# Optimization experiments

Measured on AMD Instinct MI355X. Metric: run time of the kernel, lower is better.

The kernel has to match this reference:

```python
import jax, jax.numpy as jnp
import numpy as np

D_MODEL = 2048
N_HEADS = 32
N_KV = 8
D_K = D_MODEL // N_HEADS  # 64
N_REP = N_HEADS // N_KV   # 4


def setup_inputs() -> dict:
    key = jax.random.key(0)
    ks = jax.random.split(key, 5)
    B, T = 2, 2048
    s = 0.02
    return {
        "x": jax.random.normal(ks[0], (B, T, D_MODEL), dtype=jnp.float32),
        "Wq": jax.random.normal(ks[1], (D_MODEL, D_MODEL), dtype=jnp.float32) * s,
        "Wk": jax.random.normal(ks[2], (N_KV * D_K, D_MODEL), dtype=jnp.float32) * s,
        "Wv": jax.random.normal(ks[3], (N_KV * D_K, D_MODEL), dtype=jnp.float32) * s,
        "Wo": jax.random.normal(ks[4], (D_MODEL, D_MODEL), dtype=jnp.float32) * s,
    }


def reference(x, Wq, Wk, Wv, Wo):
    B, T, C = x.shape
    # projections (torch Linear: x @ W.T)
    Q = (x @ Wq.T).reshape(B, T, N_KV, N_REP, D_K)  # group query heads by kv group
    K = (x @ Wk.T).reshape(B, T, N_KV, D_K)
    V = (x @ Wv.T).reshape(B, T, N_KV, D_K)
    scale = 1.0 / jnp.sqrt(jnp.asarray(D_K, dtype=x.dtype))
    # scores: (B, n_kv, n_rep, T, T) == repeated-KV scores without materializing repeats
    scores = jnp.einsum('btgrd,bsgd->bgrts', Q, K) * scale
    causal_mask = jnp.triu(jnp.ones((T, T), dtype=bool), k=1)
    scores = jnp.where(causal_mask, -jnp.inf, scores)
    attn = jax.nn.softmax(scores, axis=-1)
    out = jnp.einsum('bgrts,bsgd->btgrd', attn, V).reshape(B, T, C)
    return out @ Wo.T
```

## Files before the change

kernel.cpp:

```cpp
#include <hip/hip_runtime.h>
#include <hip/hip_bf16.h>

typedef __attribute__((ext_vector_type(8))) short bf16x8;
typedef __attribute__((ext_vector_type(4))) float floatx4;

constexpr int D_MODEL = 2048;
constexpr int N_HEADS = 32;
constexpr int N_KV    = 8;
constexpr int B_      = 2;
constexpr int T_      = 2048;
constexpr int BT      = B_ * T_;
constexpr int NQKV    = 3072;

constexpr float Q_SCALE = 0.18033688011112042f;

__device__ __forceinline__ unsigned short f2bf(float f) {
    __hip_bfloat16 h = __float2bfloat16(f);
    return *reinterpret_cast<unsigned short*>(&h);
}

__device__ __forceinline__ void gll16(const void* g, void* l) {
    typedef const __attribute__((address_space(1))) unsigned int* gp_t;
    typedef __attribute__((address_space(3))) unsigned int* lp_t;
    __builtin_amdgcn_global_load_lds((gp_t)g, (lp_t)l, 16, 0, 0);
}

__global__ __launch_bounds__(256) void cvt_all(
        const float* __restrict__ x,  const float* __restrict__ wq,
        const float* __restrict__ wk, const float* __restrict__ wv,
        unsigned short* __restrict__ dst) {
    size_t i4 = (size_t)blockIdx.x * 256 + threadIdx.x;
    size_t e = i4 * 4;
    const float* src; size_t off;
    if (e < 8388608)        { src = x;  off = 0; }
    else if (e < 12582912)  { src = wq; off = 8388608; }
    else if (e < 13631488)  { src = wk; off = 12582912; }
    else                    { src = wv; off = 13631488; }
    float4 f = *reinterpret_cast<const float4*>(src + (e - off));
    unsigned short u[4] = {f2bf(f.x), f2bf(f.y), f2bf(f.z), f2bf(f.w)};
    reinterpret_cast<uint2*>(dst)[i4] = *reinterpret_cast<const uint2*>(u);
}

__global__ __launch_bounds__(256) void cvt_bf16(
        const float* __restrict__ src, unsigned short* __restrict__ dst, int n4) {
    int i = blockIdx.x * 256 + threadIdx.x;
    if (i < n4) {
        float4 f = reinterpret_cast<const float4*>(src)[i];
        unsigned short u[4] = {f2bf(f.x), f2bf(f.y), f2bf(f.z), f2bf(f.w)};
        reinterpret_cast<uint2*>(dst)[i] = *reinterpret_cast<const uint2*>(u);
    }
}

template<bool C_F32, bool SCALEQ>
__global__ __launch_bounds__(256) void gemm128(
        const unsigned short* __restrict__ A,
        const unsigned short* __restrict__ Bb,
        void* __restrict__ Cp,
        int M, int N, int K) {
    __shared__ unsigned short As[128 * 64];
    __shared__ unsigned short Bs[128 * 64];
    const int t = threadIdx.x;
    const int wave = t >> 6, lane = t & 63;
    const int l16 = lane & 15, quad = lane >> 4;
    const int wm = (wave & 1) * 64, wn = (wave >> 1) * 64;
    const int mtile = blockIdx.y * 128, ntile = blockIdx.x * 128;

    floatx4 acc[4][4] = {};

    for (int k0 = 0; k0 < K; k0 += 64) {
        __syncthreads();
#pragma unroll
        for (int c = 0; c < 4; c++) {
            int s = (c * 4 + wave) * 64 + lane;
            int row = s >> 3, k8 = (s & 7) ^ (row & 7);
            gll16(&A[(size_t)(mtile + row) * K + k0 + k8 * 8], &As[(c * 4 + wave) * 512]);
            gll16(&Bb[(size_t)(ntile + row) * K + k0 + k8 * 8], &Bs[(c * 4 + wave) * 512]);
        }
        __syncthreads();
#pragma unroll
        for (int kc = 0; kc < 2; kc++) {
            bf16x8 af[4], bfr[4];
#pragma unroll
            for (int i = 0; i < 4; i++) {
                int arow = wm + i * 16 + l16;
                af[i] = *reinterpret_cast<const bf16x8*>(
                    &As[(arow * 8 + ((kc * 4 + quad) ^ (arow & 7))) * 8]);
                int brow = wn + i * 16 + l16;
                bfr[i] = *reinterpret_cast<const bf16x8*>(
                    &Bs[(brow * 8 + ((kc * 4 + quad) ^ (brow & 7))) * 8]);
            }
#pragma unroll
            for (int i = 0; i < 4; i++)
#pragma unroll
                for (int jn = 0; jn < 4; jn++)
                    acc[i][jn] = __builtin_amdgcn_mfma_f32_16x16x32_bf16(
                        af[i], bfr[jn], acc[i][jn], 0, 0, 0);
        }
    }
    float cscale = (SCALEQ && ntile < 2048) ? Q_SCALE : 1.0f;
#pragma unroll
    for (int i = 0; i < 4; i++)
#pragma unroll
        for (int jn = 0; jn < 4; jn++)
#pragma unroll
            for (int r = 0; r < 4; r++) {
                int row = mtile + wm + i * 16 + quad * 4 + r;
                int col = ntile + wn + jn * 16 + l16;
                if constexpr (C_F32)
                    ((float*)Cp)[(size_t)row * N + col] = acc[i][jn][r];
                else
                    ((unsigned short*)Cp)[(size_t)row * N + col] =
                        f2bf(acc[i][jn][r] * cscale);
            }
}

__global__ __launch_bounds__(256) void vtrans(
        const unsigned short* __restrict__ QKV,
        unsigned short* __restrict__ Vt) {
    __shared__ unsigned short Ts[64][72];
    const int tb = blockIdx.x * 64;
    const int bg = blockIdx.y;
    const int b = bg >> 3, g = bg & 7;
    const int t = threadIdx.x;
#pragma unroll
    for (int it = 0; it < 2; it++) {
        int row = (t >> 3) + it * 32;
        int sl = t & 7;
        *reinterpret_cast<uint4*>(&Ts[row][sl * 8]) =
            *reinterpret_cast<const uint4*>(
                &QKV[(size_t)(b * T_ + tb + row) * NQKV + 2560 + g * 64 + sl * 8]);
    }
    __syncthreads();
#pragma unroll
    for (int it = 0; it < 2; it++) {
        int d = (t >> 3) + it * 32;
        int ks = t & 7;
        unsigned short u[8];
#pragma unroll
        for (int j = 0; j < 8; j++) u[j] = Ts[ks * 8 + j][d];
        *reinterpret_cast<uint4*>(&Vt[((size_t)bg * 64 + d) * T_ + tb + ks * 8]) =
            *reinterpret_cast<const uint4*>(u);
    }
}

__global__ __launch_bounds__(256, 2) void attn5(
        const unsigned short* __restrict__ QKV,
        const unsigned short* __restrict__ Vt,
        unsigned short* __restrict__ O) {
    __shared__ unsigned short Ks[64 * 64];
    __shared__ unsigned short Vs[64 * 64];
    __shared__ unsigned short Ps[4][32 * 72];
    const int j  = blockIdx.x;
    const int bh = blockIdx.y;
    const int b = bh >> 5, h = bh & 31;
    const int g = h >> 2;
    const int t = threadIdx.x, wave = t >> 6, lane = t & 63;
    const int l16 = lane & 15, quad = lane >> 4;

    bf16x8 ones;
#pragma unroll
    for (int i = 0; i < 8; i++) ones[i] = (short)0x3F80;

    for (int pp = 0; pp < 2; pp++) {
        const int qtl = pp ? (15 - j) : j;
        const int q0  = qtl * 128;
        const int qlo = q0 + wave * 32;

        bf16x8 qf[2][2];
#pragma unroll
        for (int qb = 0; qb < 2; qb++) {
            const unsigned short* qptr =
                QKV + (size_t)(b * T_ + qlo + qb * 16 + l16) * NQKV + h * 64;
            qf[qb][0] = *reinterpret_cast<const bf16x8*>(qptr + quad * 8);
            qf[qb][1] = *reinterpret_cast<const bf16x8*>(qptr + 32 + quad * 8);
        }

        floatx4 o[2][4] = {};
        floatx4 lacc[2] = {};

        const int nkt = 2 * qtl + 2;
        for (int kt = 0; kt < nkt; kt++) {
            const int kb = kt * 64;
            __syncthreads();
#pragma unroll
            for (int c = 0; c < 2; c++) {
                int s = (c * 4 + wave) * 64 + lane;
                int row = s >> 3, k8 = (s & 7) ^ (row & 7);
                gll16(&QKV[(size_t)(b * T_ + kb + row) * NQKV + 2048 + g * 64 + k8 * 8],
                      &Ks[(c * 4 + wave) * 512]);
                gll16(&Vt[((size_t)(b * 8 + g) * 64 + row) * T_ + kb + k8 * 8],
                      &Vs[(c * 4 + wave) * 512]);
            }
            __syncthreads();

            if (kb > qlo + 31) continue;
            const bool needmask = (kb + 63 > qlo);

#pragma unroll
            for (int km = 0; km < 4; km++) {
                int krow = km * 16 + l16;
                bf16x8 k0 = *reinterpret_cast<const bf16x8*>(
                    &Ks[(krow * 8 + (quad ^ (krow & 7))) * 8]);
                bf16x8 k1 = *reinterpret_cast<const bf16x8*>(
                    &Ks[(krow * 8 + ((4 + quad) ^ (krow & 7))) * 8]);
#pragma unroll
                for (int qb = 0; qb < 2; qb++) {
                    floatx4 z = {};
                    z = __builtin_amdgcn_mfma_f32_16x16x32_bf16(k0, qf[qb][0], z, 0, 0, 0);
                    z = __builtin_amdgcn_mfma_f32_16x16x32_bf16(k1, qf[qb][1], z, 0, 0, 0);
                    unsigned short u[4];
                    if (needmask) {
                        int qq = qlo + qb * 16 + l16;
#pragma unroll
                        for (int r = 0; r < 4; r++) {
                            float p = __builtin_amdgcn_exp2f(z[r]);
                            if ((kb + km * 16 + quad * 4 + r) > qq) p = 0.f;
                            u[r] = f2bf(p);
                        }
                    } else {
#pragma unroll
                        for (int r = 0; r < 4; r++)
                            u[r] = f2bf(__builtin_amdgcn_exp2f(z[r]));
                    }
                    *reinterpret_cast<uint2*>(
                        &Ps[wave][(qb * 16 + l16) * 72 + km * 16 + quad * 4]) =
                        *reinterpret_cast<const uint2*>(u);
                }
            }

            bf16x8 pf[2][2];
#pragma unroll
            for (int qb = 0; qb < 2; qb++) {
#pragma unroll
                for (int ks = 0; ks < 2; ks++)
                    pf[qb][ks] = *reinterpret_cast<const bf16x8*>(
                        &Ps[wave][(qb * 16 + l16) * 72 + ks * 32 + quad * 8]);
                lacc[qb] = __builtin_amdgcn_mfma_f32_16x16x32_bf16(
                    pf[qb][0], ones, lacc[qb], 0, 0, 0);
                lacc[qb] = __builtin_amdgcn_mfma_f32_16x16x32_bf16(
                    pf[qb][1], ones, lacc[qb], 0, 0, 0);
            }
#pragma unroll
            for (int dt = 0; dt < 4; dt++) {
                int vrow = dt * 16 + l16;
                bf16x8 v0 = *reinterpret_cast<const bf16x8*>(
                    &Vs[(vrow * 8 + (quad ^ (vrow & 7))) * 8]);
                bf16x8 v1 = *reinterpret_cast<const bf16x8*>(
                    &Vs[(vrow * 8 + ((4 + quad) ^ (vrow & 7))) * 8]);
#pragma unroll
                for (int qb = 0; qb < 2; qb++) {
                    o[qb][dt] = __builtin_amdgcn_mfma_f32_16x16x32_bf16(
                        pf[qb][0], v0, o[qb][dt], 0, 0, 0);
                    o[qb][dt] = __builtin_amdgcn_mfma_f32_16x16x32_bf16(
                        pf[qb][1], v1, o[qb][dt], 0, 0, 0);
                }
            }
        }

#pragma unroll
        for (int qb = 0; qb < 2; qb++)
#pragma unroll
            for (int r = 0; r < 4; r++) {
                float inv = 1.0f / lacc[qb][r];
                int row = b * T_ + qlo + qb * 16 + quad * 4 + r;
#pragma unroll
                for (int dt = 0; dt < 4; dt++)
                    O[(size_t)row * D_MODEL + h * 64 + dt * 16 + l16] =
                        f2bf(o[qb][dt][r] * inv);
            }
    }
}

extern "C" void kernel_launch(void* const* d_in, const int* in_sizes, int n_in,
                              void* d_out, int out_size, void* d_ws, size_t ws_size,
                              hipStream_t stream) {
    const float* x  = (const float*)d_in[0];
    const float* Wq = (const float*)d_in[1];
    const float* Wk = (const float*)d_in[2];
    const float* Wv = (const float*)d_in[3];
    const float* Wo = (const float*)d_in[4];

    unsigned short* xb   = (unsigned short*)d_ws;
    unsigned short* Wqkv = xb + (size_t)BT * D_MODEL;
    unsigned short* QKVo = Wqkv + (size_t)NQKV * D_MODEL;
    unsigned short* Vt   = QKVo + (size_t)BT * NQKV;
    unsigned short* Aw   = xb;
    unsigned short* Wob  = Wqkv;

    dim3 blk(256);
    cvt_all<<<dim3(14336), blk, 0, stream>>>(x, Wq, Wk, Wv, xb);
    gemm128<false, true><<<dim3(NQKV / 128, BT / 128), blk, 0, stream>>>(
        xb, Wqkv, QKVo, BT, NQKV, D_MODEL);
    cvt_bf16<<<dim3(D_MODEL * D_MODEL / 4 / 256), blk, 0, stream>>>(
        Wo, Wob, D_MODEL * D_MODEL / 4);
    vtrans<<<dim3(T_ / 64, B_ * N_KV), blk, 0, stream>>>(QKVo, Vt);
    attn5<<<dim3(8, B_ * N_HEADS), blk, 0, stream>>>(QKVo, Vt, Aw);
    gemm128<true, false><<<dim3(D_MODEL / 128, BT / 128), blk, 0, stream>>>(
        Aw, Wob, d_out, BT, D_MODEL, D_MODEL);
}
```

Before: 275.7 us.

## Double-buffer K/V tiles in LDS and prefetch next tile during compute

Result: slower. 288.5 us (+4.6%).

```diff
diff --git a/kernel.cpp b/kernel.cpp
--- a/kernel.cpp
+++ b/kernel.cpp
@@ -147,8 +147,8 @@
         const unsigned short* __restrict__ QKV,
         const unsigned short* __restrict__ Vt,
         unsigned short* __restrict__ O) {
-    __shared__ unsigned short Ks[64 * 64];
-    __shared__ unsigned short Vs[64 * 64];
+    __shared__ unsigned short Ks[2][64 * 64];
+    __shared__ unsigned short Vs[2][64 * 64];
     __shared__ unsigned short Ps[4][32 * 72];
     const int j  = blockIdx.x;
     const int bh = blockIdx.y;
@@ -161,6 +161,19 @@
 #pragma unroll
     for (int i = 0; i < 8; i++) ones[i] = (short)0x3F80;
 
+    auto stage = [&](int kt, int bi) {
+        const int kb = kt * 64;
+#pragma unroll
+        for (int c = 0; c < 2; c++) {
+            int s = (c * 4 + wave) * 64 + lane;
+            int row = s >> 3, k8 = (s & 7) ^ (row & 7);
+            gll16(&QKV[(size_t)(b * T_ + kb + row) * NQKV + 2048 + g * 64 + k8 * 8],
+                  &Ks[bi][(c * 4 + wave) * 512]);
+            gll16(&Vt[((size_t)(b * 8 + g) * 64 + row) * T_ + kb + k8 * 8],
+                  &Vs[bi][(c * 4 + wave) * 512]);
+        }
+    };
+
     for (int pp = 0; pp < 2; pp++) {
         const int qtl = pp ? (15 - j) : j;
         const int q0  = qtl * 128;
@@ -179,82 +192,91 @@
         floatx4 lacc[2] = {};
 
         const int nkt = 2 * qtl + 2;
+        stage(0, 0);
+        int cur = 0;
         for (int kt = 0; kt < nkt; kt++) {
+            if (kt + 1 < nkt) {
+                stage(kt + 1, cur ^ 1);
+                asm volatile("s_waitcnt vmcnt(4)" ::: "memory");
+            } else {
+                asm volatile("s_waitcnt vmcnt(0)" ::: "memory");
+            }
+            __builtin_amdgcn_s_barrier();
+            asm volatile("" ::: "memory");
+
             const int kb = kt * 64;
-            __syncthreads();
-#pragma unroll
-            for (int c = 0; c < 2; c++) {
-                int s = (c * 4 + wave) * 64 + lane;
-                int row = s >> 3, k8 = (s & 7) ^ (row & 7);
-                gll16(&QKV[(size_t)(b * T_ + kb + row) * NQKV + 2048 + g * 64 + k8 * 8],
-                      &Ks[(c * 4 + wave) * 512]);
-                gll16(&Vt[((size_t)(b * 8 + g) * 64 + row) * T_ + kb + k8 * 8],
-                      &Vs[(c * 4 + wave) * 512]);
-            }
-            __syncthreads();
-
-            if (kb > qlo + 31) continue;
-            const bool needmask = (kb + 63 > qlo);
-
-#pragma unroll
-            for (int km = 0; km < 4; km++) {
-                int krow = km * 16 + l16;
-                bf16x8 k0 = *reinterpret_cast<const bf16x8*>(
-                    &Ks[(krow * 8 + (quad ^ (krow & 7))) * 8]);
-                bf16x8 k1 = *reinterpret_cast<const bf16x8*>(
-                    &Ks[(krow * 8 + ((4 + quad) ^ (krow & 7))) * 8]);
+            if (kb <= qlo + 31) {
+                const bool needmask = (kb + 63 > qlo);
+
+#pragma unroll
+                for (int km = 0; km < 4; km++) {
+                    int krow = km * 16 + l16;
+                    bf16x8 k0 = *reinterpret_cast<const bf16x8*>(
+                        &Ks[cur][(krow * 8 + (quad ^ (krow & 7))) * 8]);
+                    bf16x8 k1 = *reinterpret_cast<const bf16x8*>(
+                        &Ks[cur][(krow * 8 + ((4 + quad) ^ (krow & 7))) * 8]);
+#pragma unroll
+                    for (int qb = 0; qb < 2; qb++) {
+                        floatx4 z = {};
+                        __builtin_amdgcn_s_setprio(1);
+                        z = __builtin_amdgcn_mfma_f32_16x16x32_bf16(k0, qf[qb][0], z, 0, 0, 0);
+                        z = __builtin_amdgcn_mfma_f32_16x16x32_bf16(k1, qf[qb][1], z, 0, 0, 0);
+                        __builtin_amdgcn_s_setprio(0);
+                        unsigned short u[4];
+                        if (needmask) {
+                            int qq = qlo + qb * 16 + l16;
+#pragma unroll
+                            for (int r = 0; r < 4; r++) {
+                                float p = __builtin_amdgcn_exp2f(z[r]);
+                                if ((kb + km * 16 + quad * 4 + r) > qq) p = 0.f;
+                                u[r] = f2bf(p);
+                            }
+                        } else {
+#pragma unroll
+                            for (int r = 0; r < 4; r++)
+                                u[r] = f2bf(__builtin_amdgcn_exp2f(z[r]));
+                        }
+                        *reinterpret_cast<uint2*>(
+                            &Ps[wave][(qb * 16 + l16) * 72 + km * 16 + quad * 4]) =
+                            *reinterpret_cast<const uint2*>(u);
+                    }
+                }
+
+                bf16x8 pf[2][2];
+                __builtin_amdgcn_s_setprio(1);
 #pragma unroll
                 for (int qb = 0; qb < 2; qb++) {
-                    floatx4 z = {};
-                    z = __builtin_amdgcn_mfma_f32_16x16x32_bf16(k0, qf[qb][0], z, 0, 0, 0);
-                    z = __builtin_amdgcn_mfma_f32_16x16x32_bf16(k1, qf[qb][1], z, 0, 0, 0);
-                    unsigned short u[4];
-                    if (needmask) {
-                        int qq = qlo + qb * 16 + l16;
-#pragma unroll
-                        for (int r = 0; r < 4; r++) {
-                            float p = __builtin_amdgcn_exp2f(z[r]);
-                            if ((kb + km * 16 + quad * 4 + r) > qq) p = 0.f;
-                            u[r] = f2bf(p);
-                        }
-                    } else {
-#pragma unroll
-                        for (int r = 0; r < 4; r++)
-                            u[r] = f2bf(__builtin_amdgcn_exp2f(z[r]));
+#pragma unroll
+                    for (int ks = 0; ks < 2; ks++)
+                        pf[qb][ks] = *reinterpret_cast<const bf16x8*>(
+                            &Ps[wave][(qb * 16 + l16) * 72 + ks * 32 + quad * 8]);
+                    lacc[qb] = __builtin_amdgcn_mfma_f32_16x16x32_bf16(
+                        pf[qb][0], ones, lacc[qb], 0, 0, 0);
+                    lacc[qb] = __builtin_amdgcn_mfma_f32_16x16x32_bf16(
+                        pf[qb][1], ones, lacc[qb], 0, 0, 0);
+                }
+#pragma unroll
+                for (int dt = 0; dt < 4; dt++) {
+                    int vrow = dt * 16 + l16;
+                    bf16x8 v0 = *reinterpret_cast<const bf16x8*>(
+                        &Vs[cur][(vrow * 8 + (quad ^ (vrow & 7))) * 8]);
+                    bf16x8 v1 = *reinterpret_cast<const bf16x8*>(
+                        &Vs[cur][(vrow * 8 + ((4 + quad) ^ (vrow & 7))) * 8]);
+#pragma unroll
+                    for (int qb = 0; qb < 2; qb++) {
+                        o[qb][dt] = __builtin_amdgcn_mfma_f32_16x16x32_bf16(
+                            pf[qb][0], v0, o[qb][dt], 0, 0, 0);
+                        o[qb][dt] = __builtin_amdgcn_mfma_f32_16x16x32_bf16(
+                            pf[qb][1], v1, o[qb][dt], 0, 0, 0);
                     }
-                    *reinterpret_cast<uint2*>(
-                        &Ps[wave][(qb * 16 + l16) * 72 + km * 16 + quad * 4]) =
-                        *reinterpret_cast<const uint2*>(u);
                 }
-            }
-
-            bf16x8 pf[2][2];
-#pragma unroll
-            for (int qb = 0; qb < 2; qb++) {
-#pragma unroll
-                for (int ks = 0; ks < 2; ks++)
-                    pf[qb][ks] = *reinterpret_cast<const bf16x8*>(
-                        &Ps[wave][(qb * 16 + l16) * 72 + ks * 32 + quad * 8]);
-                lacc[qb] = __builtin_amdgcn_mfma_f32_16x16x32_bf16(
-                    pf[qb][0], ones, lacc[qb], 0, 0, 0);
-                lacc[qb] = __builtin_amdgcn_mfma_f32_16x16x32_bf16(
-                    pf[qb][1], ones, lacc[qb], 0, 0, 0);
-            }
-#pragma unroll
-            for (int dt = 0; dt < 4; dt++) {
-                int vrow = dt * 16 + l16;
-                bf16x8 v0 = *reinterpret_cast<const bf16x8*>(
-                    &Vs[(vrow * 8 + (quad ^ (vrow & 7))) * 8]);
-                bf16x8 v1 = *reinterpret_cast<const bf16x8*>(
-                    &Vs[(vrow * 8 + ((4 + quad) ^ (vrow & 7))) * 8]);
-#pragma unroll
-                for (int qb = 0; qb < 2; qb++) {
-                    o[qb][dt] = __builtin_amdgcn_mfma_f32_16x16x32_bf16(
-                        pf[qb][0], v0, o[qb][dt], 0, 0, 0);
-                    o[qb][dt] = __builtin_amdgcn_mfma_f32_16x16x32_bf16(
-                        pf[qb][1], v1, o[qb][dt], 0, 0, 0);
-                }
-            }
+                __builtin_amdgcn_s_setprio(0);
+            }
+
+            asm volatile("" ::: "memory");
+            __builtin_amdgcn_s_barrier();
+            asm volatile("" ::: "memory");
+            cur ^= 1;
         }
 
 #pragma unroll
```

## Shrink attention query tile to 64 rows per block with setprio around MFMAs

Applied to the files above, without the earlier changes.

New measurement: 289.8 us. 5.1% more time.

```diff
diff --git a/kernel.cpp b/kernel.cpp
--- a/kernel.cpp
+++ b/kernel.cpp
@@ -143,13 +143,13 @@
     }
 }
 
-__global__ __launch_bounds__(256, 2) void attn5(
+__global__ __launch_bounds__(256, 4) void attn6(
         const unsigned short* __restrict__ QKV,
         const unsigned short* __restrict__ Vt,
         unsigned short* __restrict__ O) {
     __shared__ unsigned short Ks[64 * 64];
     __shared__ unsigned short Vs[64 * 64];
-    __shared__ unsigned short Ps[4][32 * 72];
+    __shared__ unsigned short Ps[4][16 * 72];
     const int j  = blockIdx.x;
     const int bh = blockIdx.y;
     const int b = bh >> 5, h = bh & 31;
@@ -162,23 +162,19 @@
     for (int i = 0; i < 8; i++) ones[i] = (short)0x3F80;
 
     for (int pp = 0; pp < 2; pp++) {
-        const int qtl = pp ? (15 - j) : j;
-        const int q0  = qtl * 128;
-        const int qlo = q0 + wave * 32;
-
-        bf16x8 qf[2][2];
-#pragma unroll
-        for (int qb = 0; qb < 2; qb++) {
-            const unsigned short* qptr =
-                QKV + (size_t)(b * T_ + qlo + qb * 16 + l16) * NQKV + h * 64;
-            qf[qb][0] = *reinterpret_cast<const bf16x8*>(qptr + quad * 8);
-            qf[qb][1] = *reinterpret_cast<const bf16x8*>(qptr + 32 + quad * 8);
-        }
-
-        floatx4 o[2][4] = {};
-        floatx4 lacc[2] = {};
-
-        const int nkt = 2 * qtl + 2;
+        const int qtl = pp ? (31 - j) : j;
+        const int q0  = qtl * 64;
+        const int qlo = q0 + wave * 16;
+
+        const unsigned short* qptr =
+            QKV + (size_t)(b * T_ + qlo + l16) * NQKV + h * 64;
+        bf16x8 qf0 = *reinterpret_cast<const bf16x8*>(qptr + quad * 8);
+        bf16x8 qf1 = *reinterpret_cast<const bf16x8*>(qptr + 32 + quad * 8);
+
+        floatx4 o[4] = {};
+        floatx4 lacc = {};
+
+        const int nkt = qtl + 1;
         for (int kt = 0; kt < nkt; kt++) {
             const int kb = kt * 64;
             __syncthreads();
@@ -193,7 +189,7 @@
             }
             __syncthreads();
 
-            if (kb > qlo + 31) continue;
+            if (kb > qlo + 15) continue;
             const bool needmask = (kb + 63 > qlo);
 
 #pragma unroll
@@ -203,43 +199,38 @@
                     &Ks[(krow * 8 + (quad ^ (krow & 7))) * 8]);
                 bf16x8 k1 = *reinterpret_cast<const bf16x8*>(
                     &Ks[(krow * 8 + ((4 + quad) ^ (krow & 7))) * 8]);
-#pragma unroll
-                for (int qb = 0; qb < 2; qb++) {
-                    floatx4 z = {};
-                    z = __builtin_amdgcn_mfma_f32_16x16x32_bf16(k0, qf[qb][0], z, 0, 0, 0);
-                    z = __builtin_amdgcn_mfma_f32_16x16x32_bf16(k1, qf[qb][1], z, 0, 0, 0);
-                    unsigned short u[4];
-                    if (needmask) {
-                        int qq = qlo + qb * 16 + l16;
-#pragma unroll
-                        for (int r = 0; r < 4; r++) {
-                            float p = __builtin_amdgcn_exp2f(z[r]);
-                            if ((kb + km * 16 + quad * 4 + r) > qq) p = 0.f;
-                            u[r] = f2bf(p);
-                        }
-                    } else {
-#pragma unroll
-                        for (int r = 0; r < 4; r++)
-                            u[r] = f2bf(__builtin_amdgcn_exp2f(z[r]));
+                floatx4 z = {};
+                __builtin_amdgcn_s_setprio(1);
+                z = __builtin_amdgcn_mfma_f32_16x16x32_bf16(k0, qf0, z, 0, 0, 0);
+                z = __builtin_amdgcn_mfma_f32_16x16x32_bf16(k1, qf1, z, 0, 0, 0);
+                __builtin_amdgcn_s_setprio(0);
+                unsigned short u[4];
+                if (needmask) {
+                    int qq = qlo + l16;
+#pragma unroll
+                    for (int r = 0; r < 4; r++) {
+                        float p = __builtin_amdgcn_exp2f(z[r]);
+                        if ((kb + km * 16 + quad * 4 + r) > qq) p = 0.f;
+                        u[r] = f2bf(p);
                     }
-                    *reinterpret_cast<uint2*>(
-                        &Ps[wave][(qb * 16 + l16) * 72 + km * 16 + quad * 4]) =
-                        *reinterpret_cast<const uint2*>(u);
+                } else {
+#pragma unroll
+                    for (int r = 0; r < 4; r++)
+                        u[r] = f2bf(__builtin_amdgcn_exp2f(z[r]));
                 }
-            }
-
-            bf16x8 pf[2][2];
-#pragma unroll
-            for (int qb = 0; qb < 2; qb++) {
-#pragma unroll
-                for (int ks = 0; ks < 2; ks++)
-                    pf[qb][ks] = *reinterpret_cast<const bf16x8*>(
-                        &Ps[wave][(qb * 16 + l16) * 72 + ks * 32 + quad * 8]);
-                lacc[qb] = __builtin_amdgcn_mfma_f32_16x16x32_bf16(
-                    pf[qb][0], ones, lacc[qb], 0, 0, 0);
-                lacc[qb] = __builtin_amdgcn_mfma_f32_16x16x32_bf16(
-                    pf[qb][1], ones, lacc[qb], 0, 0, 0);
-            }
+                *reinterpret_cast<uint2*>(
+                    &Ps[wave][l16 * 72 + km * 16 + quad * 4]) =
+                    *reinterpret_cast<const uint2*>(u);
+            }
+
+            bf16x8 pf[2];
+            __builtin_amdgcn_s_setprio(1);
+#pragma unroll
+            for (int ks = 0; ks < 2; ks++)
+                pf[ks] = *reinterpret_cast<const bf16x8*>(
+                    &Ps[wave][l16 * 72 + ks * 32 + quad * 8]);
+            lacc = __builtin_amdgcn_mfma_f32_16x16x32_bf16(pf[0], ones, lacc, 0, 0, 0);
+            lacc = __builtin_amdgcn_mfma_f32_16x16x32_bf16(pf[1], ones, lacc, 0, 0, 0);
 #pragma unroll
             for (int dt = 0; dt < 4; dt++) {
                 int vrow = dt * 16 + l16;
@@ -247,27 +238,21 @@
                     &Vs[(vrow * 8 + (quad ^ (vrow & 7))) * 8]);
                 bf16x8 v1 = *reinterpret_cast<const bf16x8*>(
                     &Vs[(vrow * 8 + ((4 + quad) ^ (vrow & 7))) * 8]);
-#pragma unroll
-                for (int qb = 0; qb < 2; qb++) {
-                    o[qb][dt] = __builtin_amdgcn_mfma_f32_16x16x32_bf16(
-                        pf[qb][0], v0, o[qb][dt], 0, 0, 0);
-                    o[qb][dt] = __builtin_amdgcn_mfma_f32_16x16x32_bf16(
-                        pf[qb][1], v1, o[qb][dt], 0, 0, 0);
-                }
-            }
-        }
-
-#pragma unroll
-        for (int qb = 0; qb < 2; qb++)
-#pragma unroll
-            for (int r = 0; r < 4; r++) {
-                float inv = 1.0f / lacc[qb][r];
-                int row = b * T_ + qlo + qb * 16 + quad * 4 + r;
-#pragma unroll
-                for (int dt = 0; dt < 4; dt++)
-                    O[(size_t)row * D_MODEL + h * 64 + dt * 16 + l16] =
-                        f2bf(o[qb][dt][r] * inv);
-            }
+                o[dt] = __builtin_amdgcn_mfma_f32_16x16x32_bf16(pf[0], v0, o[dt], 0, 0, 0);
+                o[dt] = __builtin_amdgcn_mfma_f32_16x16x32_bf16(pf[1], v1, o[dt], 0, 0, 0);
+            }
+            __builtin_amdgcn_s_setprio(0);
+        }
+
+#pragma unroll
+        for (int r = 0; r < 4; r++) {
+            float inv = 1.0f / lacc[r];
+            int row = b * T_ + qlo + quad * 4 + r;
+#pragma unroll
+            for (int dt = 0; dt < 4; dt++)
+                O[(size_t)row * D_MODEL + h * 64 + dt * 16 + l16] =
+                    f2bf(o[dt][r] * inv);
+        }
     }
 }
 
@@ -294,7 +279,7 @@
     cvt_bf16<<<dim3(D_MODEL * D_MODEL / 4 / 256), blk, 0, stream>>>(
         Wo, Wob, D_MODEL * D_MODEL / 4);
     vtrans<<<dim3(T_ / 64, B_ * N_KV), blk, 0, stream>>>(QKVo, Vt);
-    attn5<<<dim3(8, B_ * N_HEADS), blk, 0, stream>>>(QKVo, Vt, Aw);
+    attn6<<<dim3(16, B_ * N_HEADS), blk, 0, stream>>>(QKVo, Vt, Aw);
     gemm128<true, false><<<dim3(D_MODEL / 128, BT / 128), blk, 0, stream>>>(
         Aw, Wob, d_out, BT, D_MODEL, D_MODEL);
 }
```
